# Optimization experiments

Hardware: AMD Instinct MI355X
Metric: run time of the kernel (lower is better)

Reference implementation:

```python
import jax, jax.numpy as jnp
import numpy as np

N_NODES = 50000
N_EDGES = 800000
IN_FEAT = 256
OUT_FEAT = 256
NUM_RELS = 64
NUM_BASES = 8


def setup_inputs() -> dict:
    key = jax.random.key(0)
    ks = jax.random.split(key, 9)
    x = jax.random.normal(ks[0], (N_NODES, IN_FEAT), dtype=jnp.float32)
    src = jax.random.randint(ks[1], (N_EDGES,), 0, N_NODES, dtype=jnp.int32)
    dst = jax.random.randint(ks[2], (N_EDGES,), 0, N_NODES, dtype=jnp.int32)
    etypes = jax.random.randint(ks[3], (N_EDGES,), 0, NUM_RELS, dtype=jnp.int32)
    norm = jax.random.uniform(ks[4], (N_EDGES, 1), dtype=jnp.float32)
    # glorot-style params
    s_w = (6.0 / (IN_FEAT + OUT_FEAT)) ** 0.5
    weight = jax.random.uniform(ks[5], (NUM_BASES, IN_FEAT, OUT_FEAT), jnp.float32, -s_w, s_w)
    s_c = (6.0 / (NUM_RELS + NUM_BASES)) ** 0.5
    w_comp = jax.random.uniform(ks[6], (NUM_RELS, NUM_BASES), jnp.float32, -s_c, s_c)
    h_bias = jnp.zeros((OUT_FEAT,), jnp.float32)
    loop_weight = jax.random.uniform(ks[7], (IN_FEAT, OUT_FEAT), jnp.float32, -s_w, s_w)
    return {"x": x, "src": src, "dst": dst, "etypes": etypes, "norm": norm,
            "weight": weight, "w_comp": w_comp, "h_bias": h_bias,
            "loop_weight": loop_weight}


def reference(x, src, dst, etypes, norm, weight, w_comp, h_bias, loop_weight):
    # Basis regularizer with num_bases < num_rels:
    #   W_r = sum_b w_comp[r, b] * V_b
    # Per-edge message: msg_e = (x[src_e] @ W_{etype_e}) * norm_e,
    # aggregated by sum onto destination nodes. Since the map is linear,
    # we aggregate per basis first, then apply V_b (8 dense GEMMs).
    n_nodes = x.shape[0]
    coef = w_comp[etypes]                      # [E, B] per-edge basis coeffs
    xs = x[src] * norm                         # [E, D] normalized source feats
    out = jnp.zeros((n_nodes, weight.shape[2]), x.dtype)
    for b in range(weight.shape[0]):           # small fixed loop over bases
        agg = jax.ops.segment_sum(xs * coef[:, b:b + 1], dst,
                                  num_segments=n_nodes)   # [N, D]
        out = out + agg @ weight[b]            # [N, O]
    out = out + h_bias + x @ loop_weight       # bias + self-loop
    return jax.nn.relu(out)
```

## Files before the change

kernel.cpp:

```cpp
#include <hip/hip_runtime.h>
#include <hip/hip_bf16.h>
#include <stdint.h>

#define N_NODES 50000
#define N_EDGES 800000
#define IN_FEAT 256
#define OUT_FEAT 256
#define NUM_RELS 64
#define NUM_BASES 8
#define KTOT 2304
#define KAGG 2048
#define MP 50048
#define SCAN_BLKS 196

typedef __attribute__((ext_vector_type(8))) __bf16 bf16x8;
typedef __attribute__((ext_vector_type(4))) __bf16 bf16x4;
typedef __attribute__((ext_vector_type(4))) float f32x4;
typedef __attribute__((ext_vector_type(2))) float f32x2;

static __device__ __forceinline__ void gload_lds16(const void* g, void* l) {
  auto gp = (const __attribute__((address_space(1))) void*)(uintptr_t)g;
  auto lp = (__attribute__((address_space(3))) void*)(uint32_t)(uintptr_t)l;
  __builtin_amdgcn_global_load_lds(gp, lp, 16, 0, 0);
}

__global__ void k_prex(const float* __restrict__ x, __bf16* __restrict__ xb) {
  int i = blockIdx.x * 256 + threadIdx.x;
  const float4* xp = (const float4*)x;
  float4 u = xp[i * 2], v = xp[i * 2 + 1];
  bf16x8 o;
  o[0] = (__bf16)u.x; o[1] = (__bf16)u.y; o[2] = (__bf16)u.z; o[3] = (__bf16)u.w;
  o[4] = (__bf16)v.x; o[5] = (__bf16)v.y; o[6] = (__bf16)v.z; o[7] = (__bf16)v.w;
  *(bf16x8*)(xb + (size_t)i * 8) = o;
}

__global__ void k_count(const int* __restrict__ dst, int* __restrict__ deg) {
  int e = blockIdx.x * 256 + threadIdx.x;
  atomicAdd(&deg[dst[e]], 1);
}

__global__ void k_scan1(const int* __restrict__ deg, int* __restrict__ offs,
                        int* __restrict__ bsum) {
  __shared__ int s[256];
  int t = threadIdx.x;
  int i = blockIdx.x * 256 + t;
  int v = (i < N_NODES) ? deg[i] : 0;
  s[t] = v;
  __syncthreads();
  for (int d = 1; d < 256; d <<= 1) {
    int y = (t >= d) ? s[t - d] : 0;
    __syncthreads();
    s[t] += y;
    __syncthreads();
  }
  if (i < N_NODES) offs[i] = s[t] - v;
  if (t == 255) bsum[blockIdx.x] = s[255];
}

__global__ void k_scan3(int* __restrict__ offs, const int* __restrict__ bsum,
                        int* __restrict__ fill) {
  __shared__ int s[256];
  int t = threadIdx.x;
  s[t] = (t < SCAN_BLKS && t < blockIdx.x) ? bsum[t] : 0;
  __syncthreads();
  for (int d = 128; d; d >>= 1) {
    if (t < d) s[t] += s[t + d];
    __syncthreads();
  }
  int base = s[0];
  int i = blockIdx.x * 256 + t;
  if (i < N_NODES) {
    int o = offs[i] + base;
    offs[i] = o;
    fill[i] = o;
  }
}

__global__ void k_scatter(const int* __restrict__ dst, const int* __restrict__ srcv,
                          const int* __restrict__ ety, const float* __restrict__ norm,
                          int* __restrict__ fill, uint2* __restrict__ erec) {
  int e = blockIdx.x * 256 + threadIdx.x;
  int pos = atomicAdd(&fill[dst[e]], 1);
  erec[pos] = make_uint2((unsigned)srcv[e] | ((unsigned)ety[e] << 16),
                         __float_as_uint(norm[e]));
}

__global__ __launch_bounds__(256) void k_agg(
    const __bf16* __restrict__ xb, const float* __restrict__ w_comp,
    const int* __restrict__ offs, const int* __restrict__ fin,
    const uint2* __restrict__ erec, __bf16* __restrict__ A) {
  __shared__ float wc[NUM_RELS * NUM_BASES];
  int t = threadIdx.x;
  wc[t] = w_comp[t];
  wc[t + 256] = w_comp[t + 256];
  __syncthreads();

  int wid = t >> 6, lane = t & 63;
  int node = blockIdx.x * 4 + wid;

  f32x2 acc[NUM_BASES][2];
#pragma unroll
  for (int b = 0; b < NUM_BASES; ++b) {
    acc[b][0] = f32x2{0.f, 0.f};
    acc[b][1] = f32x2{0.f, 0.f};
  }

  int i0 = offs[node];
  int cnt = fin[node] - i0;
  const uint2* rp = erec + i0;
  int lo4 = lane * 4;

  int i = 0;
  for (; i + 4 <= cnt; i += 4) {
    uint2 r[4];
#pragma unroll
    for (int j = 0; j < 4; ++j) r[j] = rp[i + j];
    uint2 xv[4];
#pragma unroll
    for (int j = 0; j < 4; ++j)
      xv[j] = *(const uint2*)(xb + (size_t)(r[j].x & 0xffff) * IN_FEAT + lo4);
#pragma unroll
    for (int j = 0; j < 4; ++j) {
      int et = r[j].x >> 16;
      float nm = __uint_as_float(r[j].y);
      f32x2 v0 = {__uint_as_float(xv[j].x << 16) * nm,
                  __uint_as_float(xv[j].x & 0xffff0000u) * nm};
      f32x2 v1 = {__uint_as_float(xv[j].y << 16) * nm,
                  __uint_as_float(xv[j].y & 0xffff0000u) * nm};
      f32x4 cl = *(const f32x4*)&wc[et * 8];
      f32x4 ch = *(const f32x4*)&wc[et * 8 + 4];
#pragma unroll
      for (int b = 0; b < 4; ++b) {
        acc[b][0] += v0 * cl[b];
        acc[b][1] += v1 * cl[b];
        acc[b + 4][0] += v0 * ch[b];
        acc[b + 4][1] += v1 * ch[b];
      }
    }
  }
  for (; i < cnt; ++i) {
    uint2 r = rp[i];
    int et = r.x >> 16;
    float nm = __uint_as_float(r.y);
    uint2 xv = *(const uint2*)(xb + (size_t)(r.x & 0xffff) * IN_FEAT + lo4);
    f32x2 v0 = {__uint_as_float(xv.x << 16) * nm,
                __uint_as_float(xv.x & 0xffff0000u) * nm};
    f32x2 v1 = {__uint_as_float(xv.y << 16) * nm,
                __uint_as_float(xv.y & 0xffff0000u) * nm};
    f32x4 cl = *(const f32x4*)&wc[et * 8];
    f32x4 ch = *(const f32x4*)&wc[et * 8 + 4];
#pragma unroll
    for (int b = 0; b < 4; ++b) {
      acc[b][0] += v0 * cl[b];
      acc[b][1] += v1 * cl[b];
      acc[b + 4][0] += v0 * ch[b];
      acc[b + 4][1] += v1 * ch[b];
    }
  }

  __bf16* Ar = A + (size_t)node * KAGG + lo4;
#pragma unroll
  for (int b = 0; b < NUM_BASES; ++b) {
    bf16x4 o;
    o[0] = (__bf16)acc[b][0][0];
    o[1] = (__bf16)acc[b][0][1];
    o[2] = (__bf16)acc[b][1][0];
    o[3] = (__bf16)acc[b][1][1];
    *(bf16x4*)(Ar + b * 256) = o;
  }
}

__global__ void k_prepw(const float* __restrict__ weight, const float* __restrict__ loop_w,
                        __bf16* __restrict__ Wt) {
  int o = blockIdx.x;
  int t = threadIdx.x;
#pragma unroll
  for (int c = 0; c < 9; ++c) {
    int r = c * 256 + t;
    float v = (r < 2048) ? weight[(size_t)r * 256 + o]
                         : loop_w[(size_t)(r - 2048) * 256 + o];
    Wt[(size_t)o * KTOT + r] = (__bf16)v;
  }
}

__global__ __launch_bounds__(256, 2) void k_gemm(const __bf16* __restrict__ A,
                                                 const __bf16* __restrict__ xb,
                                                 const __bf16* __restrict__ Wt,
                                                 const float* __restrict__ bias,
                                                 float* __restrict__ out) {
  __shared__ __align__(16) __bf16 sA[128 * 32];
  __shared__ __align__(16) __bf16 sB[256 * 32];

  int t = threadIdx.x;
  int wid = t >> 6, lane = t & 63;
  int tm = blockIdx.x;
  int wr = wid >> 1, wc = wid & 1;
  int rfw = __builtin_amdgcn_readfirstlane(wid);

  f32x4 acc[4][8];
#pragma unroll
  for (int m = 0; m < 4; ++m)
#pragma unroll
    for (int n = 0; n < 8; ++n) acc[m][n] = f32x4{0.f, 0.f, 0.f, 0.f};

  int frow = lane & 15;
  int kb = (((lane >> 4) ^ ((frow >> 1) & 3)) << 4);

  const __bf16* gaP[2];
  const __bf16* gxP[2];
#pragma unroll
  for (int it = 0; it < 2; ++it) {
    int L = it * 256 + t;
    int row = L >> 2;
    int q = (L & 3) ^ ((row >> 1) & 3);
    gaP[it] = A + (size_t)(tm * 128 + row) * KAGG + q * 8;
    gxP[it] = xb + (size_t)(tm * 128 + row) * IN_FEAT + q * 8;
  }
  const __bf16* gbP[4];
#pragma unroll
  for (int it = 0; it < 4; ++it) {
    int L = it * 256 + t;
    int row = L >> 2;
    int q = (L & 3) ^ ((row >> 1) & 3);
    gbP[it] = Wt + (size_t)row * KTOT + q * 8;
  }

#define KSTEP(A0, A1, K0)                                                   \
  do {                                                                      \
    gload_lds16((A0), (char*)sA + rfw * 1024);                              \
    gload_lds16((A1), (char*)sA + 4096 + rfw * 1024);                       \
    _Pragma("unroll") for (int it = 0; it < 4; ++it)                        \
        gload_lds16(gbP[it] + (K0), (char*)sB + (it * 256 + rfw * 64) * 16);\
    __syncthreads();                                                        \
    bf16x8 af[4], bfr[8];                                                   \
    _Pragma("unroll") for (int m = 0; m < 4; ++m)                           \
        af[m] = *(const bf16x8*)((const char*)sA +                          \
                                 (wr * 64 + m * 16 + frow) * 64 + kb);      \
    _Pragma("unroll") for (int n = 0; n < 8; ++n)                           \
        bfr[n] = *(const bf16x8*)((const char*)sB +                         \
                                  (wc * 128 + n * 16 + frow) * 64 + kb);    \
    _Pragma("unroll") for (int m = 0; m < 4; ++m)                           \
        _Pragma("unroll") for (int n = 0; n < 8; ++n)                       \
            acc[m][n] = __builtin_amdgcn_mfma_f32_16x16x32_bf16(            \
                af[m], bfr[n], acc[m][n], 0, 0, 0);                         \
    __syncthreads();                                                        \
  } while (0)

  for (int kt = 0; kt < 64; ++kt) {
    int k0 = kt * 32;
    KSTEP(gaP[0] + k0, gaP[1] + k0, k0);
  }
  for (int kt = 64; kt < 72; ++kt) {
    int k0 = kt * 32;
    int kx = k0 - KAGG;
    KSTEP(gxP[0] + kx, gxP[1] + kx, k0);
  }
#undef KSTEP

  int r0 = (lane >> 4) * 4;
  int c0 = lane & 15;
#pragma unroll
  for (int m = 0; m < 4; ++m) {
    int rowb = tm * 128 + wr * 64 + m * 16 + r0;
#pragma unroll
    for (int n = 0; n < 8; ++n) {
      int col = wc * 128 + n * 16 + c0;
      float bv = bias[col];
#pragma unroll
      for (int r = 0; r < 4; ++r) {
        int row = rowb + r;
        if (row < N_NODES) {
          float v = acc[m][n][r] + bv;
          out[(size_t)row * OUT_FEAT + col] = v > 0.f ? v : 0.f;
        }
      }
    }
  }
}

extern "C" void kernel_launch(void* const* d_in, const int* in_sizes, int n_in,
                              void* d_out, int out_size, void* d_ws, size_t ws_size,
                              hipStream_t stream) {
  const float* x      = (const float*)d_in[0];
  const int*   src    = (const int*)d_in[1];
  const int*   dst    = (const int*)d_in[2];
  const int*   ety    = (const int*)d_in[3];
  const float* norm   = (const float*)d_in[4];
  const float* weight = (const float*)d_in[5];
  const float* w_comp = (const float*)d_in[6];
  const float* h_bias = (const float*)d_in[7];
  const float* loop_w = (const float*)d_in[8];
  float* out = (float*)d_out;

  char* ws = (char*)d_ws;
  __bf16* A  = (__bf16*)ws;
  size_t off = (size_t)MP * KAGG * 2;
  __bf16* xb = (__bf16*)(ws + off);
  off += (size_t)MP * IN_FEAT * 2;
  __bf16* Wt = (__bf16*)(ws + off);
  off += (size_t)256 * KTOT * 2;
  uint2* erec = (uint2*)(ws + off);
  off += (size_t)N_EDGES * 8;
  int* deg   = (int*)(ws + off);
  int* offs  = deg + N_NODES;
  int* fill  = offs + N_NODES;
  int* bsum  = fill + N_NODES;

  hipMemsetAsync(deg, 0, N_NODES * sizeof(int), stream);
  k_prex<<<(N_NODES * IN_FEAT / 8) / 256, 256, 0, stream>>>(x, xb);
  k_count<<<N_EDGES / 256, 256, 0, stream>>>(dst, deg);
  k_scan1<<<SCAN_BLKS, 256, 0, stream>>>(deg, offs, bsum);
  k_scan3<<<SCAN_BLKS, 256, 0, stream>>>(offs, bsum, fill);
  k_scatter<<<N_EDGES / 256, 256, 0, stream>>>(dst, src, ety, norm, fill, erec);
  k_agg<<<N_NODES / 4, 256, 0, stream>>>(xb, w_comp, offs, fill, erec, A);
  k_prepw<<<256, 256, 0, stream>>>(weight, loop_w, Wt);
  k_gemm<<<MP / 128, 256, 0, stream>>>(A, xb, Wt, h_bias, out);
}
```

Before: 319.8 us.

## Double-buffer LDS tiles in GEMM to overlap global loads with MFMA

The GEMM kernel's LDS tiles for A and B are doubled, and the K loop is restructured so that the next K-slice is issued with global_load_lds into the alternate buffer while MFMAs run on the current one. This cuts synchronisation from two barriers per K-step to one and hides load latency behind compute. The cost is twice the LDS per block (48KB), which could limit occupancy alongside the existing launch bounds of 2 blocks per CU.

```diff
diff --git a/kernel.cpp b/kernel.cpp
--- a/kernel.cpp
+++ b/kernel.cpp
@@ -188,8 +188,8 @@
                                                  const __bf16* __restrict__ Wt,
                                                  const float* __restrict__ bias,
                                                  float* __restrict__ out) {
-  __shared__ __align__(16) __bf16 sA[128 * 32];
-  __shared__ __align__(16) __bf16 sB[256 * 32];
+  __shared__ __align__(16) __bf16 sA[2 * 128 * 32];
+  __shared__ __align__(16) __bf16 sB[2 * 256 * 32];
 
   int t = threadIdx.x;
   int wid = t >> 6, lane = t & 63;
@@ -225,37 +225,47 @@
     gbP[it] = Wt + (size_t)row * KTOT + q * 8;
   }
 
-#define KSTEP(A0, A1, K0)                                                   \
-  do {                                                                      \
-    gload_lds16((A0), (char*)sA + rfw * 1024);                              \
-    gload_lds16((A1), (char*)sA + 4096 + rfw * 1024);                       \
-    _Pragma("unroll") for (int it = 0; it < 4; ++it)                        \
-        gload_lds16(gbP[it] + (K0), (char*)sB + (it * 256 + rfw * 64) * 16);\
-    __syncthreads();                                                        \
-    bf16x8 af[4], bfr[8];                                                   \
-    _Pragma("unroll") for (int m = 0; m < 4; ++m)                           \
-        af[m] = *(const bf16x8*)((const char*)sA +                          \
-                                 (wr * 64 + m * 16 + frow) * 64 + kb);      \
-    _Pragma("unroll") for (int n = 0; n < 8; ++n)                           \
-        bfr[n] = *(const bf16x8*)((const char*)sB +                         \
-                                  (wc * 128 + n * 16 + frow) * 64 + kb);    \
-    _Pragma("unroll") for (int m = 0; m < 4; ++m)                           \
-        _Pragma("unroll") for (int n = 0; n < 8; ++n)                       \
-            acc[m][n] = __builtin_amdgcn_mfma_f32_16x16x32_bf16(            \
-                af[m], bfr[n], acc[m][n], 0, 0, 0);                         \
-    __syncthreads();                                                        \
+#define STAGE(KT, BUF)                                                        \
+  do {                                                                        \
+    int k0_ = (KT) * 32;                                                      \
+    const __bf16 *a0_, *a1_;                                                  \
+    if ((KT) < 64) { a0_ = gaP[0] + k0_; a1_ = gaP[1] + k0_; }                \
+    else { int kx_ = k0_ - KAGG; a0_ = gxP[0] + kx_; a1_ = gxP[1] + kx_; }    \
+    char* bA_ = (char*)sA + (BUF) * 8192;                                     \
+    char* bB_ = (char*)sB + (BUF) * 16384;                                    \
+    gload_lds16(a0_, bA_ + rfw * 1024);                                       \
+    gload_lds16(a1_, bA_ + 4096 + rfw * 1024);                                \
+    _Pragma("unroll") for (int it = 0; it < 4; ++it)                          \
+        gload_lds16(gbP[it] + k0_, bB_ + (it * 256 + rfw * 64) * 16);         \
   } while (0)
 
-  for (int kt = 0; kt < 64; ++kt) {
-    int k0 = kt * 32;
-    KSTEP(gaP[0] + k0, gaP[1] + k0, k0);
-  }
-  for (int kt = 64; kt < 72; ++kt) {
-    int k0 = kt * 32;
-    int kx = k0 - KAGG;
-    KSTEP(gxP[0] + kx, gxP[1] + kx, k0);
-  }
-#undef KSTEP
+#define COMPUTE(BUF)                                                          \
+  do {                                                                        \
+    const char* bA_ = (const char*)sA + (BUF) * 8192;                         \
+    const char* bB_ = (const char*)sB + (BUF) * 16384;                        \
+    bf16x8 af[4], bfr[8];                                                     \
+    _Pragma("unroll") for (int m = 0; m < 4; ++m)                             \
+        af[m] = *(const bf16x8*)(bA_ + (wr * 64 + m * 16 + frow) * 64 + kb);  \
+    _Pragma("unroll") for (int n = 0; n < 8; ++n)                             \
+        bfr[n] = *(const bf16x8*)(bB_ + (wc * 128 + n * 16 + frow) * 64 + kb);\
+    _Pragma("unroll") for (int m = 0; m < 4; ++m)                             \
+        _Pragma("unroll") for (int n = 0; n < 8; ++n)                         \
+            acc[m][n] = __builtin_amdgcn_mfma_f32_16x16x32_bf16(              \
+                af[m], bfr[n], acc[m][n], 0, 0, 0);                           \
+  } while (0)
+
+  STAGE(0, 0);
+  __syncthreads();
+  int cur = 0;
+  for (int kt = 0; kt < 71; ++kt) {
+    STAGE(kt + 1, cur ^ 1);
+    COMPUTE(cur);
+    __syncthreads();
+    cur ^= 1;
+  }
+  COMPUTE(cur);
+#undef STAGE
+#undef COMPUTE
 
   int r0 = (lane >> 4) * 4;
   int c0 = lane & 15;
```

New measurement: 317.2 us. About the same (-0.8%).
